# Kernel optimization log

Measured on AMD Instinct MI355X. Metric: run time of the kernel, lower is better.

## Reference

```python
import jax, jax.numpy as jnp
import numpy as np

EMBED_DIM = 128
NUM_SYMBOLS = 200000
PAD = NUM_SYMBOLS
B = 1024          # query batch
FEW = 5           # support set size
NB = 200          # neighbors per entity (fixed by module docstring)
D_MODEL = 2 * EMBED_DIM       # 256
D_INNER = 2 * D_MODEL         # 512
HID = 2 * D_MODEL             # LSTMCell hidden = 2*input_dim = 512
STEPS = 4                     # process_steps
LN_EPS = 1e-5


def setup_inputs() -> dict:
    key = jax.random.key(0)
    ks = jax.random.split(key, 16)

    def conn(k, n):
        c = jax.random.randint(k, (n, NB, 2), 0, NUM_SYMBOLS, dtype=jnp.int64)
        # pad last 50 neighbor slots so the masked max-pool path is exercised
        return c.at[:, 150:, :].set(PAD)

    inp = {
        "query_left_connections": conn(ks[0], B),
        "query_right_connections": conn(ks[1], B),
        "support_left_connections": conn(ks[2], FEW),
        "support_right_connections": conn(ks[3], FEW),
        "query_left_degrees": jax.random.randint(ks[4], (B,), 1, NB, dtype=jnp.int32),
        "query_right_degrees": jax.random.randint(ks[5], (B,), 1, NB, dtype=jnp.int32),
        "support_left_degrees": jax.random.randint(ks[6], (FEW,), 1, NB, dtype=jnp.int32),
        "support_right_degrees": jax.random.randint(ks[7], (FEW,), 1, NB, dtype=jnp.int32),
    }

    # parameters (eval mode: dropout disabled)
    emb = jax.random.normal(ks[8], (NUM_SYMBOLS + 1, EMBED_DIM), jnp.float32) * 0.02
    inp["emb"] = emb.at[PAD].set(0.0)              # padding_idx row is zero
    inp["gcn_W"] = jax.random.normal(ks[9], (EMBED_DIM, 2 * EMBED_DIM), jnp.float32) * 0.05
    inp["gcn_wb"] = jnp.zeros((EMBED_DIM,), jnp.float32)   # gcn_w linear bias
    inp["gcn_b"] = jnp.zeros((EMBED_DIM,), jnp.float32)    # extra gcn_b param (init constant 0)
    inp["proj1_W"] = jax.random.normal(ks[10], (D_INNER, D_MODEL), jnp.float32) * 0.05
    inp["proj1_b"] = jnp.zeros((D_INNER,), jnp.float32)
    inp["proj2_W"] = jax.random.normal(ks[11], (D_MODEL, D_INNER), jnp.float32) * 0.05
    inp["proj2_b"] = jnp.zeros((D_MODEL,), jnp.float32)
    inp["ln_g"] = jnp.ones((D_MODEL,), jnp.float32)
    inp["ln_b"] = jnp.zeros((D_MODEL,), jnp.float32)
    inp["W_ih"] = jax.random.normal(ks[12], (4 * HID, D_MODEL), jnp.float32) * 0.04
    inp["W_hh"] = jax.random.normal(ks[13], (4 * HID, HID), jnp.float32) * 0.04
    inp["b_ih"] = jnp.zeros((4 * HID,), jnp.float32)
    inp["b_hh"] = jnp.zeros((4 * HID,), jnp.float32)
    return inp


def _neighbor_encoder(conn, emb, gcn_W, gcn_wb, gcn_b):
    # conn: (n, NB, 2) ints; gather embed + concat + linear + leaky_relu + masked max + tanh
    rel, ent = conn[:, :, 0], conn[:, :, 1]
    pad_mask = (rel == PAD) | (ent == PAD)                      # (n, NB)
    x = jnp.concatenate([emb[rel], emb[ent]], axis=-1)          # (n, NB, 2E)
    p = jnp.einsum('nke,de->nkd', x, gcn_W) + gcn_wb + gcn_b    # (n, NB, E)
    p = jax.nn.leaky_relu(p, negative_slope=0.1)
    p = jnp.where(pad_mask[:, :, None], -jnp.inf, p)
    return jnp.tanh(jnp.max(p, axis=1))                         # (n, E)


def _support_encoder(x, p1W, p1b, p2W, p2b, g, b):
    # FFN with residual + LayerNorm (GMatching SupportEncoder), dropout off in eval
    h = jax.nn.relu(x @ p1W.T + p1b)
    o = h @ p2W.T + p2b + x
    mu = jnp.mean(o, axis=-1, keepdims=True)
    var = jnp.var(o, axis=-1, keepdims=True)
    return (o - mu) / jnp.sqrt(var + LN_EPS) * g + b


def _query_encoder(support, query, W_ih, W_hh, b_ih, b_hh):
    # GMatching QueryEncoder: LSTMCell attention, `process_steps` iterations
    # support: (1, D_MODEL), query: (bq, D_MODEL)
    bq = query.shape[0]
    h_r = jnp.zeros((bq, HID), query.dtype)
    c = jnp.zeros((bq, HID), query.dtype)
    h = query
    for _ in range(STEPS):
        gates = query @ W_ih.T + b_ih + h_r @ W_hh.T + b_hh     # (bq, 4*HID)
        i, f, g, o = jnp.split(gates, 4, axis=-1)
        c = jax.nn.sigmoid(f) * c + jax.nn.sigmoid(i) * jnp.tanh(g)
        h_new = jax.nn.sigmoid(o) * jnp.tanh(c)                 # (bq, HID)
        h = query + h_new[:, :D_MODEL]
        attn = jax.nn.softmax(h @ support.T, axis=1)            # (bq, 1)
        r = attn @ support                                      # (bq, D_MODEL)
        h_r = jnp.concatenate([h, r], axis=1)
    return h


def reference(query_left_connections, query_right_connections,
              support_left_connections, support_right_connections,
              query_left_degrees, query_right_degrees,
              support_left_degrees, support_right_degrees,
              emb, gcn_W, gcn_wb, gcn_b,
              proj1_W, proj1_b, proj2_W, proj2_b, ln_g, ln_b,
              W_ih, W_hh, b_ih, b_hh):
    ql = _neighbor_encoder(query_left_connections, emb, gcn_W, gcn_wb, gcn_b)
    qr = _neighbor_encoder(query_right_connections, emb, gcn_W, gcn_wb, gcn_b)
    sl = _neighbor_encoder(support_left_connections, emb, gcn_W, gcn_wb, gcn_b)
    sr = _neighbor_encoder(support_right_connections, emb, gcn_W, gcn_wb, gcn_b)
    query_neighbor = jnp.concatenate([ql, qr], axis=-1)      # (B, D_MODEL)
    support_neighbor = jnp.concatenate([sl, sr], axis=-1)    # (FEW, D_MODEL)

    support_g = _support_encoder(support_neighbor[None], proj1_W, proj1_b, proj2_W, proj2_b, ln_g, ln_b)
    support_g = jnp.mean(support_g, axis=1)                  # (1, D_MODEL)
    query_g = _support_encoder(query_neighbor[:, None, :], proj1_W, proj1_b, proj2_W, proj2_b, ln_g, ln_b)
    query_g = query_g[:, 0, :]                               # (B, D_MODEL)

    query_f = _query_encoder(support_g, query_g, W_ih, W_hh, b_ih, b_hh)  # (B, D_MODEL)
    return (query_f @ support_g.T)[:, 0]                     # (B,)
```

## Files before the change

kernel.cpp:

```cpp
#include <hip/hip_runtime.h>
#include <math.h>

#define EMBED   128
#define DMODEL  256
#define DINNER  512
#define HIDN    512
#define NBK     200
#define BQ      1024
#define FEW     5
#define PAD_IDX 200000
#define LN_EPS  1e-5f
#define NTILES  7

#define EMB_ELEMS 25600128
#define EMB_THREADS (EMB_ELEMS / 8)
#define EMB_BLOCKS ((EMB_THREADS + 255) / 256)

typedef short          s16x8  __attribute__((ext_vector_type(8)));
typedef float          f32x4  __attribute__((ext_vector_type(4)));
typedef float          f32x16 __attribute__((ext_vector_type(16)));
typedef unsigned int   u32;
typedef unsigned short u16;

__device__ __forceinline__ float sigmoidf_(float x) { return 1.0f / (1.0f + expf(-x)); }

__device__ __forceinline__ u32 f2bf(float f) {
    u32 u = __builtin_bit_cast(u32, f);
    u += 0x7fffu + ((u >> 16) & 1u);
    return u >> 16;
}
__device__ __forceinline__ s16x8 pack8(float4 a, float4 b) {
    typedef u32 u32x4_ __attribute__((ext_vector_type(4)));
    u32x4_ q;
    q.x = f2bf(a.x) | (f2bf(a.y) << 16);
    q.y = f2bf(a.z) | (f2bf(a.w) << 16);
    q.z = f2bf(b.x) | (f2bf(b.y) << 16);
    q.w = f2bf(b.z) | (f2bf(b.w) << 16);
    return __builtin_bit_cast(s16x8, q);
}

__global__ __launch_bounds__(256) void convert_all_kernel(
    const float* __restrict__ W_ih, const float* __restrict__ W_hh,
    const float* __restrict__ p1W,  const float* __restrict__ p2W,
    const float* __restrict__ emb,
    u16* __restrict__ wih_bf, u16* __restrict__ whh_bf,
    u16* __restrict__ p1_bf,  u16* __restrict__ p2_bf,
    u16* __restrict__ emb_bf)
{
    int bid = blockIdx.x;
    if (bid >= 512) {
        size_t gid = (size_t)(bid - 512) * 256 + threadIdx.x;
        if (gid < EMB_THREADS) {
            size_t base = gid * 8;
            float4 x0 = *(const float4*)(emb + base);
            float4 x1 = *(const float4*)(emb + base + 4);
            *(s16x8*)(emb_bf + base) = pack8(x0, x1);
        }
        return;
    }
    int gid = bid * 256 + threadIdx.x;
    const float* src; u16* dst; int local, stride, KS, liveRemap;
    if (gid < 32768)       { local = gid;          src = W_ih; dst = wih_bf; stride = 256; KS = 8;  liveRemap = 1; }
    else if (gid < 98304)  { local = gid - 32768;  src = W_hh; dst = whh_bf; stride = 512; KS = 16; liveRemap = 1; }
    else if (gid < 114688) { local = gid - 98304;  src = p1W;  dst = p1_bf;  stride = 256; KS = 8;  liveRemap = 0; }
    else                   { local = gid - 114688; src = p2W;  dst = p2_bf;  stride = 512; KS = 16; liveRemap = 0; }
    int lane = local & 63;
    int ts   = local >> 6;
    int ks   = ts & (KS - 1);
    int tile = ts / KS;
    int n  = tile * 16 + (lane & 15);
    int kb = ks * 32 + (lane >> 4) * 8;
    int row = liveRemap ? ((n >> 8) * 512 + (n & 255)) : n;
    const float* sp = src + (size_t)row * stride + kb;
    float4 x0 = *(const float4*)sp;
    float4 x1 = *(const float4*)(sp + 4);
    *(s16x8*)(dst + (size_t)local * 8) = pack8(x0, x1);
}

template<bool BF>
__global__ __launch_bounds__(256) void neighbor_kernel(
    const int* __restrict__ qlc, const int* __restrict__ qrc,
    const int* __restrict__ slc, const int* __restrict__ src_,
    const float* __restrict__ emb, const u16* __restrict__ emb_bf,
    const float* __restrict__ W,
    const float* __restrict__ wb,  const float* __restrict__ bb,
    float* __restrict__ qn, float* __restrict__ sn)
{
    int b = blockIdx.x;
    const int* conn; float* out; int n; int side;
    if (b < BQ)                { conn = qlc;  n = b;            side = 0; out = qn; }
    else if (b < 2*BQ)         { conn = qrc;  n = b - BQ;       side = 1; out = qn; }
    else if (b < 2*BQ + FEW)   { conn = slc;  n = b - 2*BQ;     side = 0; out = sn; }
    else                       { conn = src_; n = b - 2*BQ-FEW; side = 1; out = sn; }

    int t = threadIdx.x;
    int w = t >> 6, l = t & 63;
    int d0 = w * 32;
    int m31 = l & 31, half = l >> 5;

    __shared__ __align__(16) u16 bs[64 * 128];

    s16x8 afrag[16];
    const float* wrow = W + (d0 + m31) * DMODEL + half * 8;
    #pragma unroll
    for (int ks = 0; ks < 16; ++ks) {
        float4 x0 = *(const float4*)(wrow + ks * 16);
        float4 x1 = *(const float4*)(wrow + ks * 16 + 4);
        afrag[ks] = pack8(x0, x1);
    }

    const int2* crow = (const int2*)(conn + n * NBK * 2);
    u32 vmask = 0;
    #pragma unroll
    for (int nt = 0; nt < NTILES; ++nt) {
        int krow = nt * 32 + m31;
        if (krow < NBK) {
            int2 re = crow[krow];
            if (re.x != PAD_IDX && re.y != PAD_IDX) vmask |= (1u << nt);
        }
    }

    int gr = t >> 2, gq = t & 3;
    int g_m = gr & 31, g_is_ent = gr >> 5;
    int gsrc[NTILES];
    #pragma unroll
    for (int nt = 0; nt < NTILES; ++nt) {
        int krow = nt * 32 + g_m;
        int rel = PAD_IDX, ent = PAD_IDX;
        if (krow < NBK) { int2 re = crow[krow]; rel = re.x; ent = re.y; }
        int v = (rel != PAD_IDX) && (ent != PAD_IDX);
        gsrc[nt] = v ? (g_is_ent ? ent : rel) : PAD_IDX;
    }

    int tl[NTILES]; int ntl = 0;
    #pragma unroll
    for (int nt = 0; nt < NTILES; ++nt)
        if (__any((int)((vmask >> nt) & 1u))) tl[ntl++] = nt;

    float vm[16];
    #pragma unroll
    for (int r = 0; r < 16; ++r) vm[r] = -INFINITY;

    int swl = gr * 128;
    int rsw_rel = m31 * 128;
    int rsw_ent = (32 + m31) * 128;
    int rx = m31 & 15;

    s16x8 stg[4];
    auto load_tile = [&](int nt, s16x8* dstv) {
        if (BF) {
            const u16* p = emb_bf + (size_t)gsrc[nt] * EMBED + gq * 32;
            #pragma unroll
            for (int i = 0; i < 4; ++i) dstv[i] = *(const s16x8*)(p + i * 8);
        } else {
            const float* p = emb + (size_t)gsrc[nt] * EMBED + gq * 32;
            #pragma unroll
            for (int i = 0; i < 4; ++i)
                dstv[i] = pack8(*(const float4*)(p + i * 8), *(const float4*)(p + i * 8 + 4));
        }
    };

    if (ntl > 0) load_tile(tl[0], stg);

    for (int i = 0; i < ntl; ++i) {
        int nt = tl[i];
        __syncthreads();
        #pragma unroll
        for (int j = 0; j < 4; ++j) {
            int c = gq * 4 + j;
            *(s16x8*)(bs + swl + ((c ^ (gr & 15)) * 8)) = stg[j];
        }
        __syncthreads();

        s16x8 stg2[4];
        if (i + 1 < ntl) load_tile(tl[i + 1], stg2);

        f32x16 acc = {0.f,0.f,0.f,0.f,0.f,0.f,0.f,0.f,0.f,0.f,0.f,0.f,0.f,0.f,0.f,0.f};
        #pragma unroll
        for (int ks = 0; ks < 8; ++ks) {
            int c = ks * 2 + half;
            s16x8 bfr = *(const s16x8*)(bs + rsw_rel + ((c ^ rx) * 8));
            acc = __builtin_amdgcn_mfma_f32_32x32x16_bf16(afrag[ks], bfr, acc, 0, 0, 0);
        }
        #pragma unroll
        for (int ks = 0; ks < 8; ++ks) {
            int c = ks * 2 + half;
            s16x8 bfr = *(const s16x8*)(bs + rsw_ent + ((c ^ rx) * 8));
            acc = __builtin_amdgcn_mfma_f32_32x32x16_bf16(afrag[8 + ks], bfr, acc, 0, 0, 0);
        }
        int cv = (vmask >> nt) & 1;
        #pragma unroll
        for (int r = 0; r < 16; ++r) {
            float v = cv ? acc[r] : -INFINITY;
            vm[r] = fmaxf(vm[r], v);
        }
        #pragma unroll
        for (int j = 0; j < 4; ++j) stg[j] = stg2[j];
    }

    #pragma unroll
    for (int off = 1; off < 32; off <<= 1) {
        #pragma unroll
        for (int r = 0; r < 16; ++r)
            vm[r] = fmaxf(vm[r], __shfl_xor(vm[r], off, 64));
    }

    if (m31 == 0) {
        #pragma unroll
        for (int r = 0; r < 16; ++r) {
            int d = d0 + (r & 3) + 8 * (r >> 2) + 4 * half;
            float p = vm[r] + wb[d] + bb[d];
            p = (p >= 0.f) ? p : 0.1f * p;
            out[n * DMODEL + side * EMBED + d] = tanhf(p);
        }
    }
}

__global__ __launch_bounds__(512) void support_enc_kernel(
    const float* __restrict__ qn, const float* __restrict__ sn,
    const u16* __restrict__ p1_bf, const float* __restrict__ p1b,
    const u16* __restrict__ p2_bf, const float* __restrict__ p2b,
    const float* __restrict__ lng, const float* __restrict__ lnb,
    float* __restrict__ query_g, float* __restrict__ sup_ln)
{
    __shared__ __align__(16) float xs[16][260];
    __shared__ __align__(16) float hsd[16][516];
    __shared__ __align__(16) float os[16][260];
    int t = threadIdx.x;
    int w = t >> 6, l = t & 63;
    int r0 = blockIdx.x * 16;

    #pragma unroll
    for (int j = 0; j < 8; ++j) {
        int idx = j * 512 + t;
        int r = idx >> 8, cc = idx & 255;
        int row = r0 + r;
        float v = 0.f;
        if (row < BQ + FEW)
            v = (row < BQ) ? qn[(size_t)row * DMODEL + cc] : sn[(size_t)(row - BQ) * DMODEL + cc];
        xs[r][cc] = v;
    }
    __syncthreads();

    int am = l & 15, ak = (l >> 4) * 8;

    s16x8 a1[8];
    #pragma unroll
    for (int ks = 0; ks < 8; ++ks) {
        float4 x0 = *(const float4*)&xs[am][ks * 32 + ak];
        float4 x1 = *(const float4*)&xs[am][ks * 32 + ak + 4];
        a1[ks] = pack8(x0, x1);
    }

    #pragma unroll
    for (int j = 0; j < 4; ++j) {
        int nt = w * 4 + j;
        f32x4 acc = {0.f, 0.f, 0.f, 0.f};
        const u16* bp = p1_bf + (size_t)nt * 4096 + l * 8;
        #pragma unroll
        for (int ks = 0; ks < 8; ++ks) {
            s16x8 bf = *(const s16x8*)(bp + ks * 512);
            acc = __builtin_amdgcn_mfma_f32_16x16x32_bf16(a1[ks], bf, acc, 0, 0, 0);
        }
        int nn = nt * 16 + (l & 15);
        float bj = p1b[nn];
        #pragma unroll
        for (int reg = 0; reg < 4; ++reg) {
            int m = (l >> 4) * 4 + reg;
            hsd[m][nn] = fmaxf(acc[reg] + bj, 0.f);
        }
    }
    __syncthreads();

    s16x8 a2[16];
    #pragma unroll
    for (int ks = 0; ks < 16; ++ks) {
        float4 x0 = *(const float4*)&hsd[am][ks * 32 + ak];
        float4 x1 = *(const float4*)&hsd[am][ks * 32 + ak + 4];
        a2[ks] = pack8(x0, x1);
    }

    #pragma unroll
    for (int j = 0; j < 2; ++j) {
        int nt = w * 2 + j;
        f32x4 acc = {0.f, 0.f, 0.f, 0.f};
        const u16* bp = p2_bf + (size_t)nt * 8192 + l * 8;
        #pragma unroll
        for (int ks = 0; ks < 16; ++ks) {
            s16x8 bf = *(const s16x8*)(bp + ks * 512);
            acc = __builtin_amdgcn_mfma_f32_16x16x32_bf16(a2[ks], bf, acc, 0, 0, 0);
        }
        int nn = nt * 16 + (l & 15);
        float bj = p2b[nn];
        #pragma unroll
        for (int reg = 0; reg < 4; ++reg) {
            int m = (l >> 4) * 4 + reg;
            os[m][nn] = acc[reg] + bj + xs[m][nn];
        }
    }
    __syncthreads();

    for (int j = 0; j < 2; ++j) {
        int m = w * 2 + j;
        float sum = 0.f, sq = 0.f;
        #pragma unroll
        for (int i = 0; i < 4; ++i) {
            float v = os[m][l + 64 * i];
            sum += v; sq += v * v;
        }
        for (int off = 32; off; off >>= 1) {
            sum += __shfl_xor(sum, off, 64);
            sq  += __shfl_xor(sq,  off, 64);
        }
        float mu  = sum * (1.f / DMODEL);
        float var = sq * (1.f / DMODEL) - mu * mu;
        float inv = rsqrtf(var + LN_EPS);
        int row = r0 + m;
        if (row < BQ + FEW) {
            float* outp = (row < BQ) ? (query_g + (size_t)row * DMODEL) : (sup_ln + (size_t)(row - BQ) * DMODEL);
            #pragma unroll
            for (int i = 0; i < 4; ++i) {
                int dd = l + 64 * i;
                outp[dd] = (os[m][dd] - mu) * inv * lng[dd] + lnb[dd];
            }
        }
    }
}

__global__ __launch_bounds__(512) void lstm_mfma_kernel(
    const float* __restrict__ query_g, const float* __restrict__ sup_ln,
    const u16* __restrict__ wih_bf, const u16* __restrict__ whh_bf,
    const float* __restrict__ b_ih, const float* __restrict__ b_hh,
    float* __restrict__ out)
{
    __shared__ __align__(16) float qs[16][260];
    __shared__ __align__(16) float hq[16][516];
    int t = threadIdx.x;
    int w = t >> 6, l = t & 63;
    int n0 = blockIdx.x * 16;

    {
        int cc = t & 255;
        float a = 0.f;
        for (int i = 0; i < FEW; ++i) a += sup_ln[i * DMODEL + cc];
        float svv = a * (1.f / FEW);
        #pragma unroll
        for (int j = 0; j < 8; ++j) {
            int idx = j * 512 + t;
            int r = idx >> 8;
            qs[r][cc] = query_g[(size_t)(n0 + r) * DMODEL + cc];
            hq[r][256 + cc] = svv;
        }
    }
    __syncthreads();

    int am = l & 15, ak = (l >> 4) * 8;

    f32x4 base[4][2];
    {
        s16x8 af[8];
        #pragma unroll
        for (int ks = 0; ks < 8; ++ks) {
            float4 x0 = *(const float4*)&qs[am][ks * 32 + ak];
            float4 x1 = *(const float4*)&qs[am][ks * 32 + ak + 4];
            af[ks] = pack8(x0, x1);
        }
        #pragma unroll
        for (int pp = 0; pp < 4; ++pp) {
            #pragma unroll
            for (int qt = 0; qt < 2; ++qt) {
                int tp = pp * 16 + 2 * w + qt;
                f32x4 acc = {0.f, 0.f, 0.f, 0.f};
                const u16* bp = wih_bf + (size_t)tp * 4096 + l * 8;
                #pragma unroll
                for (int ks = 0; ks < 8; ++ks) {
                    s16x8 bf = *(const s16x8*)(bp + ks * 512);
                    acc = __builtin_amdgcn_mfma_f32_16x16x32_bf16(af[ks], bf, acc, 0, 0, 0);
                }
                base[pp][qt] = acc;
            }
        }
    }
    #pragma unroll
    for (int pp = 0; pp < 4; ++pp) {
        #pragma unroll
        for (int qt = 0; qt < 2; ++qt) {
            int q = w * 32 + qt * 16 + (l & 15);
            float bsv = b_ih[pp * 512 + q] + b_hh[pp * 512 + q];
            base[pp][qt].x += bsv; base[pp][qt].y += bsv;
            base[pp][qt].z += bsv; base[pp][qt].w += bsv;
        }
    }

    float c[2][4];
    #pragma unroll
    for (int qt = 0; qt < 2; ++qt) {
        int q = w * 32 + qt * 16 + (l & 15);
        #pragma unroll
        for (int reg = 0; reg < 4; ++reg) {
            int m = (l >> 4) * 4 + reg;
            float gi = base[0][qt][reg];
            float gg = base[2][qt][reg];
            float go = base[3][qt][reg];
            float cc = sigmoidf_(gi) * tanhf(gg);
            c[qt][reg] = cc;
            hq[m][q] = qs[m][q] + sigmoidf_(go) * tanhf(cc);
        }
    }
    __syncthreads();

    for (int st = 1; st < 4; ++st) {
        s16x8 af[16];
        #pragma unroll
        for (int ks = 0; ks < 16; ++ks) {
            float4 x0 = *(const float4*)&hq[am][ks * 32 + ak];
            float4 x1 = *(const float4*)&hq[am][ks * 32 + ak + 4];
            af[ks] = pack8(x0, x1);
        }
        __syncthreads();

        f32x4 gacc[4][2];
        #pragma unroll
        for (int pp = 0; pp < 4; ++pp) {
            #pragma unroll
            for (int qt = 0; qt < 2; ++qt) {
                int tp = pp * 16 + 2 * w + qt;
                f32x4 acc = base[pp][qt];
                const u16* bp = whh_bf + (size_t)tp * 8192 + l * 8;
                #pragma unroll
                for (int ks = 0; ks < 16; ++ks) {
                    s16x8 bf = *(const s16x8*)(bp + ks * 512);
                    acc = __builtin_amdgcn_mfma_f32_16x16x32_bf16(af[ks], bf, acc, 0, 0, 0);
                }
                gacc[pp][qt] = acc;
            }
        }
        #pragma unroll
        for (int qt = 0; qt < 2; ++qt) {
            int q = w * 32 + qt * 16 + (l & 15);
            #pragma unroll
            for (int reg = 0; reg < 4; ++reg) {
                int m = (l >> 4) * 4 + reg;
                float gi = gacc[0][qt][reg];
                float gf = gacc[1][qt][reg];
                float gg = gacc[2][qt][reg];
                float go = gacc[3][qt][reg];
                float cc = sigmoidf_(gf) * c[qt][reg] + sigmoidf_(gi) * tanhf(gg);
                c[qt][reg] = cc;
                hq[m][q] = qs[m][q] + sigmoidf_(go) * tanhf(cc);
            }
        }
        __syncthreads();
    }

    for (int j = 0; j < 2; ++j) {
        int m = w * 2 + j;
        float part = 0.f;
        #pragma unroll
        for (int i = 0; i < 4; ++i) {
            int e = l + 64 * i;
            part += hq[m][e] * hq[m][256 + e];
        }
        for (int off = 32; off; off >>= 1) part += __shfl_xor(part, off, 64);
        if (l == 0) out[n0 + m] = part;
    }
}

extern "C" void kernel_launch(void* const* d_in, const int* in_sizes, int n_in,
                              void* d_out, int out_size, void* d_ws, size_t ws_size,
                              hipStream_t stream)
{
    const int*   qlc  = (const int*)d_in[0];
    const int*   qrc  = (const int*)d_in[1];
    const int*   slc  = (const int*)d_in[2];
    const int*   src_ = (const int*)d_in[3];
    const float* emb   = (const float*)d_in[8];
    const float* gcnW  = (const float*)d_in[9];
    const float* gcnwb = (const float*)d_in[10];
    const float* gcnb  = (const float*)d_in[11];
    const float* p1W   = (const float*)d_in[12];
    const float* p1b   = (const float*)d_in[13];
    const float* p2W   = (const float*)d_in[14];
    const float* p2b   = (const float*)d_in[15];
    const float* lng   = (const float*)d_in[16];
    const float* lnb   = (const float*)d_in[17];
    const float* W_ih  = (const float*)d_in[18];
    const float* W_hh  = (const float*)d_in[19];
    const float* b_ih  = (const float*)d_in[20];
    const float* b_hh  = (const float*)d_in[21];
    float* out = (float*)d_out;

    char* ws = (char*)d_ws;
    float* qn      = (float*)(ws + 0);
    float* sn      = (float*)(ws + 1048576);
    float* query_g = (float*)(ws + 1053696);
    float* sup_ln  = (float*)(ws + 2102272);
    u16*   wih_bf  = (u16*)(ws + 2107392);
    u16*   whh_bf  = (u16*)(ws + 2631680);
    u16*   p1_bf   = (u16*)(ws + 3680256);
    u16*   p2_bf   = (u16*)(ws + 3942400);
    u16*   emb_bf  = (u16*)(ws + 4204544);
    (void)in_sizes; (void)n_in; (void)out_size;

    bool have_emb = ws_size >= (size_t)4204544 + (size_t)EMB_ELEMS * 2;
    int grid_conv = 512 + (have_emb ? EMB_BLOCKS : 0);

    convert_all_kernel<<<grid_conv, 256, 0, stream>>>(
        W_ih, W_hh, p1W, p2W, emb, wih_bf, whh_bf, p1_bf, p2_bf, emb_bf);
    if (have_emb)
        neighbor_kernel<true><<<2 * BQ + 2 * FEW, 256, 0, stream>>>(
            qlc, qrc, slc, src_, emb, emb_bf, gcnW, gcnwb, gcnb, qn, sn);
    else
        neighbor_kernel<false><<<2 * BQ + 2 * FEW, 256, 0, stream>>>(
            qlc, qrc, slc, src_, emb, emb_bf, gcnW, gcnwb, gcnb, qn, sn);
    support_enc_kernel<<<(BQ + FEW + 15) / 16, 512, 0, stream>>>(
        qn, sn, p1_bf, p1b, p2_bf, p2b, lng, lnb, query_g, sup_ln);
    lstm_mfma_kernel<<<BQ / 16, 512, 0, stream>>>(
        query_g, sup_ln, wih_bf, whh_bf, b_ih, b_hh, out);
}
```

Before: 423.4 us.

## Split encoder and LSTM into grid-wide GEMM kernels, precompute support half of W_hh

Breaks the fused support encoder and LSTM into separate GEMM, layernorm, and per-step kernels tiled across many more blocks. The hidden state's second half is always the constant support vector, so its W_hh product is computed once as a per-gate bias (sWp), halving the recurrent GEMM K dimension. Only the query half of W_hh is converted to bf16. This raises parallelism but adds launches and global round-trips for intermediates (h1, o_g, base_g, c, h).

```diff
diff --git a/kernel.cpp b/kernel.cpp
--- a/kernel.cpp
+++ b/kernel.cpp
@@ -11,6 +11,7 @@
 #define PAD_IDX 200000
 #define LN_EPS  1e-5f
 #define NTILES  7
+#define MPAD    1056
 
 #define EMB_ELEMS 25600128
 #define EMB_THREADS (EMB_ELEMS / 8)
@@ -48,8 +49,8 @@
     u16* __restrict__ emb_bf)
 {
     int bid = blockIdx.x;
-    if (bid >= 512) {
-        size_t gid = (size_t)(bid - 512) * 256 + threadIdx.x;
+    if (bid >= 384) {
+        size_t gid = (size_t)(bid - 384) * 256 + threadIdx.x;
         if (gid < EMB_THREADS) {
             size_t base = gid * 8;
             float4 x0 = *(const float4*)(emb + base);
@@ -60,10 +61,10 @@
     }
     int gid = bid * 256 + threadIdx.x;
     const float* src; u16* dst; int local, stride, KS, liveRemap;
-    if (gid < 32768)       { local = gid;          src = W_ih; dst = wih_bf; stride = 256; KS = 8;  liveRemap = 1; }
-    else if (gid < 98304)  { local = gid - 32768;  src = W_hh; dst = whh_bf; stride = 512; KS = 16; liveRemap = 1; }
-    else if (gid < 114688) { local = gid - 98304;  src = p1W;  dst = p1_bf;  stride = 256; KS = 8;  liveRemap = 0; }
-    else                   { local = gid - 114688; src = p2W;  dst = p2_bf;  stride = 512; KS = 16; liveRemap = 0; }
+    if (gid < 32768)      { local = gid;          src = W_ih; dst = wih_bf; stride = 256; KS = 8;  liveRemap = 1; }
+    else if (gid < 65536) { local = gid - 32768;  src = W_hh; dst = whh_bf; stride = 512; KS = 8;  liveRemap = 1; }
+    else if (gid < 81920) { local = gid - 65536;  src = p1W;  dst = p1_bf;  stride = 256; KS = 8;  liveRemap = 0; }
+    else                  { local = gid - 81920;  src = p2W;  dst = p2_bf;  stride = 512; KS = 16; liveRemap = 0; }
     int lane = local & 63;
     int ts   = local >> 6;
     int ks   = ts & (KS - 1);
@@ -216,253 +217,285 @@
     }
 }
 
-__global__ __launch_bounds__(512) void support_enc_kernel(
+__device__ __forceinline__ const float* xrow_ptr(
+    const float* qn, const float* sn, int row) {
+    if (row < BQ) return qn + (size_t)row * DMODEL;
+    if (row < BQ + FEW) return sn + (size_t)(row - BQ) * DMODEL;
+    return nullptr;
+}
+
+__global__ __launch_bounds__(256) void gemm1_kernel(
     const float* __restrict__ qn, const float* __restrict__ sn,
     const u16* __restrict__ p1_bf, const float* __restrict__ p1b,
-    const u16* __restrict__ p2_bf, const float* __restrict__ p2b,
-    const float* __restrict__ lng, const float* __restrict__ lnb,
-    float* __restrict__ query_g, float* __restrict__ sup_ln)
-{
-    __shared__ __align__(16) float xs[16][260];
-    __shared__ __align__(16) float hsd[16][516];
-    __shared__ __align__(16) float os[16][260];
-    int t = threadIdx.x;
-    int w = t >> 6, l = t & 63;
-    int r0 = blockIdx.x * 16;
-
-    #pragma unroll
-    for (int j = 0; j < 8; ++j) {
-        int idx = j * 512 + t;
-        int r = idx >> 8, cc = idx & 255;
-        int row = r0 + r;
-        float v = 0.f;
-        if (row < BQ + FEW)
-            v = (row < BQ) ? qn[(size_t)row * DMODEL + cc] : sn[(size_t)(row - BQ) * DMODEL + cc];
-        xs[r][cc] = v;
-    }
-    __syncthreads();
-
+    u16* __restrict__ h1_bf)
+{
+    int bid = blockIdx.x;
+    int mb = bid % 33, nb = bid / 33;
+    int m0 = mb * 32, n0 = nb * 64;
+    int t = threadIdx.x, w = t >> 6, l = t & 63;
+    int msub = w & 1, npair = w >> 1;
     int am = l & 15, ak = (l >> 4) * 8;
 
-    s16x8 a1[8];
+    int arow = m0 + msub * 16 + am;
+    const float* xr = xrow_ptr(qn, sn, arow);
+    s16x8 af[8];
     #pragma unroll
     for (int ks = 0; ks < 8; ++ks) {
-        float4 x0 = *(const float4*)&xs[am][ks * 32 + ak];
-        float4 x1 = *(const float4*)&xs[am][ks * 32 + ak + 4];
-        a1[ks] = pack8(x0, x1);
-    }
-
-    #pragma unroll
-    for (int j = 0; j < 4; ++j) {
-        int nt = w * 4 + j;
+        float4 x0 = {0.f,0.f,0.f,0.f}, x1 = {0.f,0.f,0.f,0.f};
+        if (xr) { x0 = *(const float4*)(xr + ks * 32 + ak); x1 = *(const float4*)(xr + ks * 32 + ak + 4); }
+        af[ks] = pack8(x0, x1);
+    }
+
+    #pragma unroll
+    for (int j = 0; j < 2; ++j) {
+        int nt = (n0 >> 4) + npair * 2 + j;
         f32x4 acc = {0.f, 0.f, 0.f, 0.f};
         const u16* bp = p1_bf + (size_t)nt * 4096 + l * 8;
         #pragma unroll
         for (int ks = 0; ks < 8; ++ks) {
             s16x8 bf = *(const s16x8*)(bp + ks * 512);
-            acc = __builtin_amdgcn_mfma_f32_16x16x32_bf16(a1[ks], bf, acc, 0, 0, 0);
+            acc = __builtin_amdgcn_mfma_f32_16x16x32_bf16(af[ks], bf, acc, 0, 0, 0);
         }
         int nn = nt * 16 + (l & 15);
         float bj = p1b[nn];
         #pragma unroll
         for (int reg = 0; reg < 4; ++reg) {
-            int m = (l >> 4) * 4 + reg;
-            hsd[m][nn] = fmaxf(acc[reg] + bj, 0.f);
-        }
-    }
-    __syncthreads();
-
-    s16x8 a2[16];
-    #pragma unroll
-    for (int ks = 0; ks < 16; ++ks) {
-        float4 x0 = *(const float4*)&hsd[am][ks * 32 + ak];
-        float4 x1 = *(const float4*)&hsd[am][ks * 32 + ak + 4];
-        a2[ks] = pack8(x0, x1);
-    }
+            int mg = m0 + msub * 16 + (l >> 4) * 4 + reg;
+            float v = fmaxf(acc[reg] + bj, 0.f);
+            h1_bf[(size_t)mg * DINNER + nn] = (u16)f2bf(v);
+        }
+    }
+}
+
+__global__ __launch_bounds__(256) void gemm2_kernel(
+    const u16* __restrict__ h1_bf, const u16* __restrict__ p2_bf,
+    const float* __restrict__ p2b, const float* __restrict__ qn,
+    const float* __restrict__ sn, float* __restrict__ o_g)
+{
+    int bid = blockIdx.x;
+    int mb = bid % 33, nb = bid / 33;
+    int m0 = mb * 32, n0 = nb * 64;
+    int t = threadIdx.x, w = t >> 6, l = t & 63;
+    int msub = w & 1, npair = w >> 1;
+    int am = l & 15, ak = (l >> 4) * 8;
+
+    int arow = m0 + msub * 16 + am;
+    s16x8 af[16];
+    #pragma unroll
+    for (int ks = 0; ks < 16; ++ks)
+        af[ks] = *(const s16x8*)(h1_bf + (size_t)arow * DINNER + ks * 32 + ak);
 
     #pragma unroll
     for (int j = 0; j < 2; ++j) {
-        int nt = w * 2 + j;
+        int nt = (n0 >> 4) + npair * 2 + j;
         f32x4 acc = {0.f, 0.f, 0.f, 0.f};
         const u16* bp = p2_bf + (size_t)nt * 8192 + l * 8;
         #pragma unroll
         for (int ks = 0; ks < 16; ++ks) {
             s16x8 bf = *(const s16x8*)(bp + ks * 512);
-            acc = __builtin_amdgcn_mfma_f32_16x16x32_bf16(a2[ks], bf, acc, 0, 0, 0);
+            acc = __builtin_amdgcn_mfma_f32_16x16x32_bf16(af[ks], bf, acc, 0, 0, 0);
         }
         int nn = nt * 16 + (l & 15);
         float bj = p2b[nn];
         #pragma unroll
         for (int reg = 0; reg < 4; ++reg) {
-            int m = (l >> 4) * 4 + reg;
-            os[m][nn] = acc[reg] + bj + xs[m][nn];
-        }
-    }
-    __syncthreads();
-
+            int mg = m0 + msub * 16 + (l >> 4) * 4 + reg;
+            const float* xr = xrow_ptr(qn, sn, mg);
+            float res = xr ? xr[nn] : 0.f;
+            o_g[(size_t)mg * DMODEL + nn] = acc[reg] + bj + res;
+        }
+    }
+}
+
+__global__ __launch_bounds__(256) void ln_kernel(
+    const float* __restrict__ o_g, const float* __restrict__ lng,
+    const float* __restrict__ lnb, float* __restrict__ query_g,
+    float* __restrict__ sup_ln)
+{
+    int t = threadIdx.x, w = t >> 6, l = t & 63;
+    int row = blockIdx.x * 4 + w;
+    if (row >= BQ + FEW) return;
+    const float* op = o_g + (size_t)row * DMODEL;
+    float v[4], sum = 0.f, sq = 0.f;
+    #pragma unroll
+    for (int i = 0; i < 4; ++i) {
+        v[i] = op[l + 64 * i];
+        sum += v[i]; sq += v[i] * v[i];
+    }
+    for (int off = 32; off; off >>= 1) {
+        sum += __shfl_xor(sum, off, 64);
+        sq  += __shfl_xor(sq,  off, 64);
+    }
+    float mu  = sum * (1.f / DMODEL);
+    float var = sq * (1.f / DMODEL) - mu * mu;
+    float inv = rsqrtf(var + LN_EPS);
+    float* outp = (row < BQ) ? (query_g + (size_t)row * DMODEL)
+                             : (sup_ln + (size_t)(row - BQ) * DMODEL);
+    #pragma unroll
+    for (int i = 0; i < 4; ++i) {
+        int dd = l + 64 * i;
+        outp[dd] = (v[i] - mu) * inv * lng[dd] + lnb[dd];
+    }
+}
+
+__global__ __launch_bounds__(256) void sWp_kernel(
+    const float* __restrict__ sup_ln, const float* __restrict__ W_hh,
+    float* __restrict__ sWp, float* __restrict__ s_vec)
+{
+    int w = threadIdx.x >> 6, l = threadIdx.x & 63;
+    int wave_id = blockIdx.x * 4 + w;
+    float se[4];
+    #pragma unroll
+    for (int j = 0; j < 4; ++j) {
+        float a = 0.f;
+        for (int i = 0; i < FEW; ++i) a += sup_ln[i * DMODEL + l + 64 * j];
+        se[j] = a * (1.f / FEW);
+    }
+    if (blockIdx.x == 0 && w == 0) {
+        #pragma unroll
+        for (int j = 0; j < 4; ++j) s_vec[l + 64 * j] = se[j];
+    }
+    for (int i = 0; i < 4; ++i) {
+        int p = wave_id * 4 + i;
+        int pp = p >> 8, q = p & 255;
+        const float* wr = W_hh + (size_t)(pp * 512 + q) * HIDN + 256;
+        float part = 0.f;
+        #pragma unroll
+        for (int j = 0; j < 4; ++j) part += se[j] * wr[l + 64 * j];
+        for (int off = 32; off; off >>= 1) part += __shfl_xor(part, off, 64);
+        if (l == 0) sWp[p] = part;
+    }
+}
+
+__global__ __launch_bounds__(256) void base_kernel(
+    const float* __restrict__ query_g, const u16* __restrict__ wih_bf,
+    const float* __restrict__ b_ih, const float* __restrict__ b_hh,
+    float* __restrict__ base_g)
+{
+    int bid = blockIdx.x;
+    int mb = bid & 31, nb = bid >> 5;
+    int m0 = mb * 32, n0 = nb * 64;
+    int t = threadIdx.x, w = t >> 6, l = t & 63;
+    int msub = w & 1, npair = w >> 1;
+    int am = l & 15, ak = (l >> 4) * 8;
+
+    int arow = m0 + msub * 16 + am;
+    const float* xr = query_g + (size_t)arow * DMODEL;
+    s16x8 af[8];
+    #pragma unroll
+    for (int ks = 0; ks < 8; ++ks)
+        af[ks] = pack8(*(const float4*)(xr + ks * 32 + ak),
+                       *(const float4*)(xr + ks * 32 + ak + 4));
+
+    #pragma unroll
     for (int j = 0; j < 2; ++j) {
-        int m = w * 2 + j;
-        float sum = 0.f, sq = 0.f;
-        #pragma unroll
-        for (int i = 0; i < 4; ++i) {
-            float v = os[m][l + 64 * i];
-            sum += v; sq += v * v;
-        }
-        for (int off = 32; off; off >>= 1) {
-            sum += __shfl_xor(sum, off, 64);
-            sq  += __shfl_xor(sq,  off, 64);
-        }
-        float mu  = sum * (1.f / DMODEL);
-        float var = sq * (1.f / DMODEL) - mu * mu;
-        float inv = rsqrtf(var + LN_EPS);
-        int row = r0 + m;
-        if (row < BQ + FEW) {
-            float* outp = (row < BQ) ? (query_g + (size_t)row * DMODEL) : (sup_ln + (size_t)(row - BQ) * DMODEL);
-            #pragma unroll
-            for (int i = 0; i < 4; ++i) {
-                int dd = l + 64 * i;
-                outp[dd] = (os[m][dd] - mu) * inv * lng[dd] + lnb[dd];
-            }
-        }
-    }
-}
-
-__global__ __launch_bounds__(512) void lstm_mfma_kernel(
-    const float* __restrict__ query_g, const float* __restrict__ sup_ln,
-    const u16* __restrict__ wih_bf, const u16* __restrict__ whh_bf,
-    const float* __restrict__ b_ih, const float* __restrict__ b_hh,
+        int nt = (n0 >> 4) + npair * 2 + j;
+        f32x4 acc = {0.f, 0.f, 0.f, 0.f};
+        const u16* bp = wih_bf + (size_t)nt * 4096 + l * 8;
+        #pragma unroll
+        for (int ks = 0; ks < 8; ++ks) {
+            s16x8 bf = *(const s16x8*)(bp + ks * 512);
+            acc = __builtin_amdgcn_mfma_f32_16x16x32_bf16(af[ks], bf, acc, 0, 0, 0);
+        }
+        int p = nt * 16 + (l & 15);
+        int pp = p >> 8, q = p & 255;
+        float bsv = b_ih[pp * 512 + q] + b_hh[pp * 512 + q];
+        #pragma unroll
+        for (int reg = 0; reg < 4; ++reg) {
+            int mg = m0 + msub * 16 + (l >> 4) * 4 + reg;
+            base_g[(size_t)mg * 1024 + p] = acc[reg] + bsv;
+        }
+    }
+}
+
+__global__ __launch_bounds__(256) void step0_kernel(
+    const float* __restrict__ base_g, const float* __restrict__ query_g,
+    float* __restrict__ c_g, float* __restrict__ h_out)
+{
+    int m = blockIdx.x, q = threadIdx.x;
+    const float* bm = base_g + (size_t)m * 1024;
+    float gi = bm[q];
+    float gg = bm[512 + q];
+    float go = bm[768 + q];
+    float cc = sigmoidf_(gi) * tanhf(gg);
+    c_g[(size_t)m * DMODEL + q] = cc;
+    h_out[(size_t)m * DMODEL + q] = query_g[(size_t)m * DMODEL + q]
+                                  + sigmoidf_(go) * tanhf(cc);
+}
+
+__global__ __launch_bounds__(256) void step_kernel(
+    const float* __restrict__ h_prev, const float* __restrict__ base_g,
+    const float* __restrict__ sWp, const u16* __restrict__ whh_bf,
+    const float* __restrict__ query_g, float* __restrict__ c_g,
+    float* __restrict__ h_next)
+{
+    int bid = blockIdx.x;
+    int mb = bid & 31, qb = bid >> 5;
+    int m0 = mb * 32, q0 = qb * 32;
+    int t = threadIdx.x, w = t >> 6, l = t & 63;
+    int msub = w & 1, qsub = w >> 1;
+    int am = l & 15, ak = (l >> 4) * 8;
+
+    int arow = m0 + msub * 16 + am;
+    const float* hr = h_prev + (size_t)arow * DMODEL;
+    s16x8 af[8];
+    #pragma unroll
+    for (int ks = 0; ks < 8; ++ks)
+        af[ks] = pack8(*(const float4*)(hr + ks * 32 + ak),
+                       *(const float4*)(hr + ks * 32 + ak + 4));
+
+    int qq = q0 + qsub * 16 + (l & 15);
+    f32x4 gacc[4];
+    #pragma unroll
+    for (int pp = 0; pp < 4; ++pp) {
+        int tp = pp * 16 + qb * 2 + qsub;
+        float sw = sWp[pp * 256 + qq];
+        f32x4 acc;
+        #pragma unroll
+        for (int reg = 0; reg < 4; ++reg) {
+            int mg = m0 + msub * 16 + (l >> 4) * 4 + reg;
+            acc[reg] = base_g[(size_t)mg * 1024 + pp * 256 + qq] + sw;
+        }
+        const u16* bp = whh_bf + (size_t)tp * 4096 + l * 8;
+        #pragma unroll
+        for (int ks = 0; ks < 8; ++ks) {
+            s16x8 bf = *(const s16x8*)(bp + ks * 512);
+            acc = __builtin_amdgcn_mfma_f32_16x16x32_bf16(af[ks], bf, acc, 0, 0, 0);
+        }
+        gacc[pp] = acc;
+    }
+
+    #pragma unroll
+    for (int reg = 0; reg < 4; ++reg) {
+        int mg = m0 + msub * 16 + (l >> 4) * 4 + reg;
+        float gi = gacc[0][reg];
+        float gf = gacc[1][reg];
+        float gg = gacc[2][reg];
+        float go = gacc[3][reg];
+        size_t idx = (size_t)mg * DMODEL + qq;
+        float cold = c_g[idx];
+        float cc = sigmoidf_(gf) * cold + sigmoidf_(gi) * tanhf(gg);
+        c_g[idx] = cc;
+        h_next[idx] = query_g[idx] + sigmoidf_(go) * tanhf(cc);
+    }
+}
+
+__global__ __launch_bounds__(256) void final_kernel(
+    const float* __restrict__ h_st, const float* __restrict__ s_vec,
     float* __restrict__ out)
 {
-    __shared__ __align__(16) float qs[16][260];
-    __shared__ __align__(16) float hq[16][516];
-    int t = threadIdx.x;
-    int w = t >> 6, l = t & 63;
-    int n0 = blockIdx.x * 16;
-
-    {
-        int cc = t & 255;
-        float a = 0.f;
-        for (int i = 0; i < FEW; ++i) a += sup_ln[i * DMODEL + cc];
-        float svv = a * (1.f / FEW);
-        #pragma unroll
-        for (int j = 0; j < 8; ++j) {
-            int idx = j * 512 + t;
-            int r = idx >> 8;
-            qs[r][cc] = query_g[(size_t)(n0 + r) * DMODEL + cc];
-            hq[r][256 + cc] = svv;
-        }
-    }
-    __syncthreads();
-
-    int am = l & 15, ak = (l >> 4) * 8;
-
-    f32x4 base[4][2];
-    {
-        s16x8 af[8];
-        #pragma unroll
-        for (int ks = 0; ks < 8; ++ks) {
-            float4 x0 = *(const float4*)&qs[am][ks * 32 + ak];
-            float4 x1 = *(const float4*)&qs[am][ks * 32 + ak + 4];
-            af[ks] = pack8(x0, x1);
-        }
-        #pragma unroll
-        for (int pp = 0; pp < 4; ++pp) {
-            #pragma unroll
-            for (int qt = 0; qt < 2; ++qt) {
-                int tp = pp * 16 + 2 * w + qt;
-                f32x4 acc = {0.f, 0.f, 0.f, 0.f};
-                const u16* bp = wih_bf + (size_t)tp * 4096 + l * 8;
-                #pragma unroll
-                for (int ks = 0; ks < 8; ++ks) {
-                    s16x8 bf = *(const s16x8*)(bp + ks * 512);
-                    acc = __builtin_amdgcn_mfma_f32_16x16x32_bf16(af[ks], bf, acc, 0, 0, 0);
-                }
-                base[pp][qt] = acc;
-            }
-        }
-    }
-    #pragma unroll
-    for (int pp = 0; pp < 4; ++pp) {
-        #pragma unroll
-        for (int qt = 0; qt < 2; ++qt) {
-            int q = w * 32 + qt * 16 + (l & 15);
-            float bsv = b_ih[pp * 512 + q] + b_hh[pp * 512 + q];
-            base[pp][qt].x += bsv; base[pp][qt].y += bsv;
-            base[pp][qt].z += bsv; base[pp][qt].w += bsv;
-        }
-    }
-
-    float c[2][4];
-    #pragma unroll
-    for (int qt = 0; qt < 2; ++qt) {
-        int q = w * 32 + qt * 16 + (l & 15);
-        #pragma unroll
-        for (int reg = 0; reg < 4; ++reg) {
-            int m = (l >> 4) * 4 + reg;
-            float gi = base[0][qt][reg];
-            float gg = base[2][qt][reg];
-            float go = base[3][qt][reg];
-            float cc = sigmoidf_(gi) * tanhf(gg);
-            c[qt][reg] = cc;
-            hq[m][q] = qs[m][q] + sigmoidf_(go) * tanhf(cc);
-        }
-    }
-    __syncthreads();
-
-    for (int st = 1; st < 4; ++st) {
-        s16x8 af[16];
-        #pragma unroll
-        for (int ks = 0; ks < 16; ++ks) {
-            float4 x0 = *(const float4*)&hq[am][ks * 32 + ak];
-            float4 x1 = *(const float4*)&hq[am][ks * 32 + ak + 4];
-            af[ks] = pack8(x0, x1);
-        }
-        __syncthreads();
-
-        f32x4 gacc[4][2];
-        #pragma unroll
-        for (int pp = 0; pp < 4; ++pp) {
-            #pragma unroll
-            for (int qt = 0; qt < 2; ++qt) {
-                int tp = pp * 16 + 2 * w + qt;
-                f32x4 acc = base[pp][qt];
-                const u16* bp = whh_bf + (size_t)tp * 8192 + l * 8;
-                #pragma unroll
-                for (int ks = 0; ks < 16; ++ks) {
-                    s16x8 bf = *(const s16x8*)(bp + ks * 512);
-                    acc = __builtin_amdgcn_mfma_f32_16x16x32_bf16(af[ks], bf, acc, 0, 0, 0);
-                }
-                gacc[pp][qt] = acc;
-            }
-        }
-        #pragma unroll
-        for (int qt = 0; qt < 2; ++qt) {
-            int q = w * 32 + qt * 16 + (l & 15);
-            #pragma unroll
-            for (int reg = 0; reg < 4; ++reg) {
-                int m = (l >> 4) * 4 + reg;
-                float gi = gacc[0][qt][reg];
-                float gf = gacc[1][qt][reg];
-                float gg = gacc[2][qt][reg];
-                float go = gacc[3][qt][reg];
-                float cc = sigmoidf_(gf) * c[qt][reg] + sigmoidf_(gi) * tanhf(gg);
-                c[qt][reg] = cc;
-                hq[m][q] = qs[m][q] + sigmoidf_(go) * tanhf(cc);
-            }
-        }
-        __syncthreads();
-    }
-
-    for (int j = 0; j < 2; ++j) {
-        int m = w * 2 + j;
+    int w = threadIdx.x >> 6, l = threadIdx.x & 63;
+    int wave_id = blockIdx.x * 4 + w;
+    for (int i = 0; i < 16; ++i) {
+        int n = wave_id * 16 + i;
         float part = 0.f;
         #pragma unroll
-        for (int i = 0; i < 4; ++i) {
-            int e = l + 64 * i;
-            part += hq[m][e] * hq[m][256 + e];
+        for (int j = 0; j < 4; ++j) {
+            int e = l + 64 * j;
+            part += h_st[(size_t)n * DMODEL + e] * s_vec[e];
         }
         for (int off = 32; off; off >>= 1) part += __shfl_xor(part, off, 64);
-        if (l == 0) out[n0 + m] = part;
+        if (l == 0) out[n] = part;
     }
 }
 
@@ -495,15 +528,23 @@
     float* sn      = (float*)(ws + 1048576);
     float* query_g = (float*)(ws + 1053696);
     float* sup_ln  = (float*)(ws + 2102272);
-    u16*   wih_bf  = (u16*)(ws + 2107392);
-    u16*   whh_bf  = (u16*)(ws + 2631680);
-    u16*   p1_bf   = (u16*)(ws + 3680256);
-    u16*   p2_bf   = (u16*)(ws + 3942400);
-    u16*   emb_bf  = (u16*)(ws + 4204544);
+    float* s_vec   = (float*)(ws + 2107392);
+    float* sWp     = (float*)(ws + 2108416);
+    u16*   wih_bf  = (u16*)(ws + 2112512);
+    u16*   whh_bf  = (u16*)(ws + 2636800);
+    u16*   p1_bf   = (u16*)(ws + 3161088);
+    u16*   p2_bf   = (u16*)(ws + 3423232);
+    u16*   h1_bf   = (u16*)(ws + 3685376);
+    float* o_g     = (float*)(ws + 4766720);
+    float* base_g  = (float*)(ws + 5848064);
+    float* c_g     = (float*)(ws + 10042368);
+    float* h_a     = (float*)(ws + 11090944);
+    float* h_b     = (float*)(ws + 12139520);
+    u16*   emb_bf  = (u16*)(ws + 13188096);
     (void)in_sizes; (void)n_in; (void)out_size;
 
-    bool have_emb = ws_size >= (size_t)4204544 + (size_t)EMB_ELEMS * 2;
-    int grid_conv = 512 + (have_emb ? EMB_BLOCKS : 0);
+    bool have_emb = ws_size >= (size_t)13188096 + (size_t)EMB_ELEMS * 2;
+    int grid_conv = 384 + (have_emb ? EMB_BLOCKS : 0);
 
     convert_all_kernel<<<grid_conv, 256, 0, stream>>>(
         W_ih, W_hh, p1W, p2W, emb, wih_bf, whh_bf, p1_bf, p2_bf, emb_bf);
@@ -513,8 +554,16 @@
     else
         neighbor_kernel<false><<<2 * BQ + 2 * FEW, 256, 0, stream>>>(
             qlc, qrc, slc, src_, emb, emb_bf, gcnW, gcnwb, gcnb, qn, sn);
-    support_enc_kernel<<<(BQ + FEW + 15) / 16, 512, 0, stream>>>(
-        qn, sn, p1_bf, p1b, p2_bf, p2b, lng, lnb, query_g, sup_ln);
-    lstm_mfma_kernel<<<BQ / 16, 512, 0, stream>>>(
-        query_g, sup_ln, wih_bf, whh_bf, b_ih, b_hh, out);
-}
+
+    gemm1_kernel<<<33 * 8, 256, 0, stream>>>(qn, sn, p1_bf, p1b, h1_bf);
+    gemm2_kernel<<<33 * 4, 256, 0, stream>>>(h1_bf, p2_bf, p2b, qn, sn, o_g);
+    ln_kernel<<<258, 256, 0, stream>>>(o_g, lng, lnb, query_g, sup_ln);
+    sWp_kernel<<<64, 256, 0, stream>>>(sup_ln, W_hh, sWp, s_vec);
+
+    base_kernel<<<512, 256, 0, stream>>>(query_g, wih_bf, b_ih, b_hh, base_g);
+    step0_kernel<<<1024, 256, 0, stream>>>(base_g, query_g, c_g, h_a);
+    step_kernel<<<256, 256, 0, stream>>>(h_a, base_g, sWp, whh_bf, query_g, c_g, h_b);
+    step_kernel<<<256, 256, 0, stream>>>(h_b, base_g, sWp, whh_bf, query_g, c_g, h_a);
+    step_kernel<<<256, 256, 0, stream>>>(h_a, base_g, sWp, whh_bf, query_g, c_g, h_b);
+    final_kernel<<<16, 256, 0, stream>>>(h_b, s_vec, out);
+}
```

Measured after the change: 341.9 us. -19.2%, faster.
